# Kernel tuning notes

Measured on AMD Instinct MI355X. Metric: run time of the kernel, lower is better.

## Reference

```python
import jax, jax.numpy as jnp
import numpy as np

T, B, E, H, F = 1024, 2, 1024, 16, 8
D = E // H
R = 2 * T - 1  # relative positions T-1 .. -(T-1)


def setup_inputs() -> dict:
    key = jax.random.key(0)
    ks = jax.random.split(key, 11)
    std = float(np.sqrt(2.0 / (E + E)))
    return {
        "input": jax.random.normal(ks[0], (T, B, E), jnp.float32),
        "pos": jax.random.normal(ks[1], (R, B, E), jnp.float32),
        "factor": jax.random.normal(ks[2], (F,), jnp.float32),
        "in_proj_weight": jax.random.normal(ks[3], (3 * E * E, F), jnp.float32) * std,
        "pos_proj_weight": jax.random.normal(ks[4], (E * E, F), jnp.float32) * std,
        "out_proj_weight": jax.random.normal(ks[5], (E * E, F), jnp.float32) * std,
        "in_proj_bias": jax.random.normal(ks[6], (3 * E, F), jnp.float32) * 0.02,
        "pos_proj_bias": jax.random.normal(ks[7], (E, F), jnp.float32) * 0.02,
        "out_proj_bias": jax.random.normal(ks[8], (E, F), jnp.float32) * 0.02,
        "r_w_bias": jax.random.normal(ks[9], (E, F), jnp.float32) * 0.02,
        "r_r_bias": jax.random.normal(ks[10], (E, F), jnp.float32) * 0.02,
    }


def _rel_shift(x):
    # x: [BH, T, R] -> out[b, i, j] = x[b, i, j + (T-1) - i]
    bh, q, r = x.shape
    zp = jnp.zeros((bh, q, 1), x.dtype)
    xp = jnp.concatenate([zp, x], axis=2).reshape(bh, r + 1, q)
    return xp[:, 1:, :].reshape(bh, q, r)


def reference(input, pos, factor, in_proj_weight, pos_proj_weight, out_proj_weight,
              in_proj_bias, pos_proj_bias, out_proj_bias, r_w_bias, r_r_bias):
    # hypernetwork: generate effective weights from factor vector (torch.mv)
    W_in = (in_proj_weight @ factor).reshape(3 * E, E)
    W_pos = (pos_proj_weight @ factor).reshape(E, E)
    W_out = (out_proj_weight @ factor).reshape(E, E)
    b_in = in_proj_bias @ factor
    b_pos = pos_proj_bias @ factor
    b_out = out_proj_bias @ factor
    rw = (r_w_bias @ factor).reshape(H, D)  # content bias
    rr = (r_r_bias @ factor).reshape(H, D)  # position bias

    qkv = input @ W_in.T + b_in                      # [T, B, 3E]
    q, k, v = jnp.split(qkv, 3, axis=-1)
    q = q.reshape(T, B, H, D)
    k = k.reshape(T, B, H, D)
    v = v.reshape(T, B, H, D)
    r = (pos @ W_pos.T + b_pos).reshape(R, B, H, D)  # [R, B, H, D]

    scale = 1.0 / np.sqrt(D)
    # AC: content-content + content bias term
    AC = jnp.einsum('ibhd,jbhd->bhij', q + rw, k)    # [B, H, T, T]
    # BD: content-position + position bias term, then relative shift
    BD = jnp.einsum('ibhd,rbhd->bhir', q + rr, r)    # [B, H, T, R]
    BD = _rel_shift(BD.reshape(B * H, T, R))[:, :, :T].reshape(B, H, T, T)

    attn = jax.nn.softmax((AC + BD) * scale, axis=-1)  # [B, H, T, T]
    out = jnp.einsum('bhij,jbhd->ibhd', attn, v).reshape(T, B, E)
    out = out @ W_out.T + b_out                       # [T, B, E]
    return out
```

## Files before the change

kernel.cpp:

```cpp
#include <hip/hip_runtime.h>


typedef _Float16 h16;
typedef _Float16 h16x8 __attribute__((ext_vector_type(8)));
typedef _Float16 h16x4 __attribute__((ext_vector_type(4)));
typedef float f32x4 __attribute__((ext_vector_type(4)));

static __device__ __forceinline__ f32x4 mfma16(h16x8 a, h16x8 b, f32x4 c) {
  return __builtin_amdgcn_mfma_f32_16x16x32_f16(a, b, c, 0, 0, 0);
}
static __device__ __forceinline__ void gload16(const void* g, void* l) {
  __builtin_amdgcn_global_load_lds((const __attribute__((address_space(1))) void*)g,
                                   (__attribute__((address_space(3))) void*)l, 16, 0, 0);
}

__global__ __launch_bounds__(256, 2) void hypernet_kernel(
    const float* __restrict__ fac,
    const float* __restrict__ w_in, const float* __restrict__ w_pos,
    const float* __restrict__ w_out, const float* __restrict__ b_in_w,
    const float* __restrict__ b_pos_w, const float* __restrict__ b_out_w,
    const float* __restrict__ rw_w, const float* __restrict__ rr_w,
    h16* __restrict__ Wall,
    float* __restrict__ bin, float* __restrict__ bpos, float* __restrict__ bout,
    float* __restrict__ rw, float* __restrict__ rr, h16* __restrict__ rb,
    const float* __restrict__ input, const float* __restrict__ pos,
    h16* __restrict__ cast_h)
{
  const int tid = threadIdx.x;
  const float f0=fac[0],f1=fac[1],f2=fac[2],f3=fac[3],
              f4=fac[4],f5=fac[5],f6=fac[6],f7=fac[7];
#define DOT(a,b) ((a).x*f0+(a).y*f1+(a).z*f2+(a).w*f3+(b).x*f4+(b).y*f5+(b).z*f6+(b).w*f7)

  if (blockIdx.x < 1280) {
    const int b = blockIdx.x;
    const float* tbl; size_t rowbase;
    if (b < 768)       { tbl = w_in;  rowbase = (size_t)b*4096; }
    else if (b < 1024) { tbl = w_pos; rowbase = (size_t)b*4096 - 3145728; }
    else               { tbl = w_out; rowbase = (size_t)b*4096 - 4194304; }
    const size_t outbase = (size_t)b*4096;
    float4 cur[4], nxt[4];
    {
      const float4* p0 = reinterpret_cast<const float4*>(tbl + (rowbase + tid)*8);
      const float4* p1 = reinterpret_cast<const float4*>(tbl + (rowbase + 256 + tid)*8);
      cur[0]=p0[0]; cur[1]=p0[1]; cur[2]=p1[0]; cur[3]=p1[1];
    }
#pragma unroll
    for (int s = 0; s < 8; ++s) {
      if (s < 7) {
        const float4* p0 = reinterpret_cast<const float4*>(tbl + (rowbase + (s+1)*512 + tid)*8);
        const float4* p1 = reinterpret_cast<const float4*>(tbl + (rowbase + (s+1)*512 + 256 + tid)*8);
        nxt[0]=p0[0]; nxt[1]=p0[1]; nxt[2]=p1[0]; nxt[3]=p1[1];
      }
      Wall[outbase + s*512 + tid]       = (h16)DOT(cur[0], cur[1]);
      Wall[outbase + s*512 + 256 + tid] = (h16)DOT(cur[2], cur[3]);
#pragma unroll
      for (int q = 0; q < 4; ++q) cur[q] = nxt[q];
    }
    return;
  }
  if (blockIdx.x < 1316) {
    int idx = (blockIdx.x - 1280) * 256 + tid;
    if (idx < 3072) {
      const float4* s = reinterpret_cast<const float4*>(b_in_w + (size_t)idx*8);
      bin[idx] = DOT(s[0], s[1]); return;
    }
    idx -= 3072;
    if (idx < 1024) {
      const float4* s = reinterpret_cast<const float4*>(b_pos_w + (size_t)idx*8);
      bpos[idx] = DOT(s[0], s[1]); return;
    }
    idx -= 1024;
    if (idx < 1024) {
      const float4* s = reinterpret_cast<const float4*>(b_out_w + (size_t)idx*8);
      bout[idx] = DOT(s[0], s[1]); return;
    }
    idx -= 1024;
    if (idx < 1024) {
      const float4* s = reinterpret_cast<const float4*>(rw_w + (size_t)idx*8);
      rw[idx] = DOT(s[0], s[1]); return;
    }
    idx -= 1024;
    if (idx < 1024) {
      const float4* s = reinterpret_cast<const float4*>(rr_w + (size_t)idx*8);
      rr[idx] = DOT(s[0], s[1]); return;
    }
    idx -= 1024;
    if (idx < 2048)
      rb[(((size_t)(idx >> 6)) << 17) + 2047*64 + (idx & 63)] = (h16)0.f;
    return;
  }
  {
    const int g = (blockIdx.x - 1316) * 256 + tid;
    float4 v = (g < 524288) ? reinterpret_cast<const float4*>(input)[g]
                            : reinterpret_cast<const float4*>(pos)[g - 524288];
    h16x4 o = { (h16)v.x, (h16)v.y, (h16)v.z, (h16)v.w };
    reinterpret_cast<h16x4*>(cast_h)[g] = o;
  }
#undef DOT
}

template <int MODE>
__global__ __launch_bounds__(256) void gemm_lds_kernel(
    const h16* __restrict__ A, const h16* __restrict__ Bw,
    const float* __restrict__ bias, int M, int N, int K,
    float* __restrict__ Cout,
    const float* __restrict__ rwv, const float* __restrict__ rrv,
    h16* __restrict__ o0, h16* __restrict__ o1,
    h16* __restrict__ o2, h16* __restrict__ o3)
{
  __shared__ __align__(16) h16 a_sm[128*64];
  __shared__ __align__(16) h16 b_sm[128*64];
  const int tid = threadIdx.x, lane = tid & 63, wave = tid >> 6;
  const int quad = lane >> 4, t16 = lane & 15;
  const int wm = wave >> 1, wn = wave & 1;
  const int m0 = blockIdx.y * 128, n0 = blockIdx.x * 128;
  const int lrow = lane >> 3, lgran = lane & 7;
  const int gsw = (lgran ^ lrow) * 8;
  const int xg0 = (quad ^ (t16 & 7)) * 8;
  const int xg1 = xg0 ^ 32;

  f32x4 acc[4][4];
#pragma unroll
  for (int i = 0; i < 4; ++i)
#pragma unroll
    for (int j = 0; j < 4; ++j) acc[i][j] = (f32x4){0.f,0.f,0.f,0.f};

  for (int k0 = 0; k0 < K; k0 += 64) {
    __syncthreads();
#pragma unroll
    for (int s = 0; s < 4; ++s) {
      int rbase = wave*32 + s*8;
      gload16(A  + (size_t)(m0 + rbase + lrow)*K + k0 + gsw, a_sm + rbase*64);
      gload16(Bw + (size_t)(n0 + rbase + lrow)*K + k0 + gsw, b_sm + rbase*64);
    }
    __syncthreads();
#pragma unroll
    for (int kc = 0; kc < 2; ++kc) {
      const int xg = kc ? xg1 : xg0;
      h16x8 af[4], bfr[4];
#pragma unroll
      for (int i = 0; i < 4; ++i) {
        af[i]  = *reinterpret_cast<const h16x8*>(a_sm + (wm*64 + i*16 + t16)*64 + xg);
        bfr[i] = *reinterpret_cast<const h16x8*>(b_sm + (wn*64 + i*16 + t16)*64 + xg);
      }
#pragma unroll
      for (int i = 0; i < 4; ++i)
#pragma unroll
        for (int j = 0; j < 4; ++j)
          acc[i][j] = mfma16(af[i], bfr[j], acc[i][j]);
    }
  }

#pragma unroll
  for (int i = 0; i < 4; ++i) {
    int mb = m0 + wm*64 + i*16 + quad*4;
#pragma unroll
    for (int j = 0; j < 4; ++j) {
      int n = n0 + wn*64 + j*16 + t16;
      float bv = bias[n];
      if (MODE == 2) {
#pragma unroll
        for (int r = 0; r < 4; ++r)
          Cout[(size_t)(mb + r)*N + n] = acc[i][j][r] + bv;
      } else if (MODE == 0) {
        int nn = n & 1023, sec = n >> 10, hh = nn >> 6, d = nn & 63;
        float rwb = rwv[nn], rrb = rrv[nn];
#pragma unroll
        for (int r = 0; r < 4; ++r) {
          int m = mb + r, t = m >> 1, b = m & 1;
          size_t off = ((size_t)((b << 4) + hh) << 16) + (t << 6) + d;
          float v = acc[i][j][r] + bv;
          if (sec == 0)      { o0[off] = (h16)(v + rwb); o1[off] = (h16)(v + rrb); }
          else if (sec == 1) { o2[off] = (h16)v; }
          else               { o3[off] = (h16)v; }
        }
      } else {
        int hh = n >> 6, d = n & 63;
#pragma unroll
        for (int r = 0; r < 4; ++r) {
          int m = mb + r;
          if (m < M) {
            int rel = m >> 1, b = m & 1;
            o0[(((size_t)((b << 4) + hh)) << 17) + (rel << 6) + d] = (h16)(acc[i][j][r] + bv);
          }
        }
      }
    }
  }
}

__global__ __launch_bounds__(256) void transpose_v_kernel(
    const h16* __restrict__ vb, h16* __restrict__ vbt)
{
  __shared__ h16 tile[64*72];
  const int bh = blockIdx.y, t0 = blockIdx.x * 64;
  const int r = threadIdx.x >> 3, c = (threadIdx.x & 7) * 8;
  const h16* src = vb + ((size_t)bh << 16) + (size_t)(t0 + r)*64 + c;
  *reinterpret_cast<h16x8*>(tile + r*72 + c)        = *reinterpret_cast<const h16x8*>(src);
  *reinterpret_cast<h16x8*>(tile + (r + 32)*72 + c) = *reinterpret_cast<const h16x8*>(src + 32*64);
  __syncthreads();
  h16x8 o0, o1;
#pragma unroll
  for (int e = 0; e < 8; ++e) {
    o0[e] = tile[(c + e)*72 + r];
    o1[e] = tile[(c + e)*72 + r + 32];
  }
  h16* dst = vbt + ((size_t)bh << 16) + (size_t)r*1024 + t0 + c;
  *reinterpret_cast<h16x8*>(dst)            = o0;
  *reinterpret_cast<h16x8*>(dst + 32*1024)  = o1;
}

__global__ __launch_bounds__(256) void flash_kernel(
    const h16* __restrict__ qrw, const h16* __restrict__ qrr,
    const h16* __restrict__ kb, const h16* __restrict__ vbt,
    const h16* __restrict__ rb,
    float* __restrict__ o_part, float* __restrict__ ml_part)
{
  __shared__ __align__(16) h16 k_sm[64*64];
  __shared__ __align__(16) h16 vt_sm[64*64];
  __shared__ __align__(16) h16 r_sm[128*64];

  const int tid = threadIdx.x, lane = tid & 63, wave = tid >> 6;
  const int quad = lane >> 4, t16 = lane & 15;
  const int bh = blockIdx.y, i0 = blockIdx.x * 64, jh = blockIdx.z;
  const size_t base  = (size_t)bh << 16;
  const size_t rbase = (size_t)bh << 17;
  const int iw = i0 + wave * 16;
  const int lrow = lane >> 3, lgran = lane & 7;
  const int gsw = (lgran ^ lrow) * 8;
  const int xg0 = (quad ^ (t16 & 7)) * 8;
  const int xg1 = xg0 ^ 32;

  h16x8 a_rw[2], a_rr[2];
  {
    const h16* p = qrw + base + (size_t)(iw + t16)*64 + quad*8;
    a_rw[0] = *reinterpret_cast<const h16x8*>(p);
    a_rw[1] = *reinterpret_cast<const h16x8*>(p + 32);
    const h16* p2 = qrr + base + (size_t)(iw + t16)*64 + quad*8;
    a_rr[0] = *reinterpret_cast<const h16x8*>(p2);
    a_rr[1] = *reinterpret_cast<const h16x8*>(p2 + 32);
  }

  f32x4 o_acc[4];
#pragma unroll
  for (int dc = 0; dc < 4; ++dc) o_acc[dc] = (f32x4){0.f,0.f,0.f,0.f};
  float m_run[4] = {-1e30f,-1e30f,-1e30f,-1e30f};
  float l_run[4] = {0.f,0.f,0.f,0.f};

  h16* bdw = r_sm + wave * (16*84);
  const int cb0 = 3 - wave;

  for (int j0 = jh*256; j0 < jh*256 + 256; j0 += 64) {
    __syncthreads();
    {
#pragma unroll
      for (int s = 0; s < 2; ++s) {
        int row = wave*16 + s*8;
        gload16(kb  + base + (size_t)(j0 + row + lrow)*64 + gsw, k_sm  + row*64);
        gload16(vbt + base + (size_t)(row + lrow)*1024 + j0 + gsw, vt_sm + row*64);
      }
      const int rel0 = j0 - i0 + 960;
#pragma unroll
      for (int s = 0; s < 4; ++s) {
        int row = wave*32 + s*8;
        gload16(rb + rbase + (size_t)(rel0 + row + lrow)*64 + gsw, r_sm + row*64);
      }
    }
    __syncthreads();

    f32x4 s_ac[4];
#pragma unroll
    for (int c = 0; c < 4; ++c) {
      s_ac[c] = (f32x4){0.f,0.f,0.f,0.f};
      s_ac[c] = mfma16(a_rw[0], *reinterpret_cast<const h16x8*>(k_sm + (c*16 + t16)*64 + xg0), s_ac[c]);
      s_ac[c] = mfma16(a_rw[1], *reinterpret_cast<const h16x8*>(k_sm + (c*16 + t16)*64 + xg1), s_ac[c]);
    }
    f32x4 s_bd[5];
#pragma unroll
    for (int u = 0; u < 5; ++u) {
      s_bd[u] = (f32x4){0.f,0.f,0.f,0.f};
      s_bd[u] = mfma16(a_rr[0], *reinterpret_cast<const h16x8*>(r_sm + ((cb0+u)*16 + t16)*64 + xg0), s_bd[u]);
      s_bd[u] = mfma16(a_rr[1], *reinterpret_cast<const h16x8*>(r_sm + ((cb0+u)*16 + t16)*64 + xg1), s_bd[u]);
    }
    __syncthreads();

#pragma unroll
    for (int u = 0; u < 5; ++u)
#pragma unroll
      for (int r = 0; r < 4; ++r)
        bdw[(quad*4 + r)*84 + u*16 + t16] = (h16)s_bd[u][r];

    float sv[4][4];
#pragma unroll
    for (int c = 0; c < 4; ++c)
#pragma unroll
      for (int r = 0; r < 4; ++r) {
        int il = quad*4 + r;
        float bdv = (float)bdw[il*84 + c*16 + t16 + 15 - il];
        sv[c][r] = (s_ac[c][r] + bdv) * 0.125f;
      }

    float alpha[4];
#pragma unroll
    for (int r = 0; r < 4; ++r) {
      float v = fmaxf(fmaxf(sv[0][r], sv[1][r]), fmaxf(sv[2][r], sv[3][r]));
#pragma unroll
      for (int off = 1; off < 16; off <<= 1) v = fmaxf(v, __shfl_xor(v, off, 64));
      float mn = fmaxf(m_run[r], v);
      alpha[r] = __expf(m_run[r] - mn);
      m_run[r] = mn;
    }
#pragma unroll
    for (int r = 0; r < 4; ++r) {
      float s0 = 0.f;
#pragma unroll
      for (int c = 0; c < 4; ++c) {
        float p = __expf(sv[c][r] - m_run[r]);
        sv[c][r] = p; s0 += p;
      }
      l_run[r] = l_run[r]*alpha[r] + s0;
    }
#pragma unroll
    for (int dc = 0; dc < 4; ++dc) {
      f32x4 t = o_acc[dc];
#pragma unroll
      for (int r = 0; r < 4; ++r) t[r] *= alpha[r];
      o_acc[dc] = t;
    }
    h16* pw = bdw;
#pragma unroll
    for (int c = 0; c < 4; ++c)
#pragma unroll
      for (int r = 0; r < 4; ++r)
        pw[(quad*4 + r)*72 + c*16 + t16] = (h16)sv[c][r];

    h16x8 ap0 = *reinterpret_cast<const h16x8*>(pw + t16*72 + quad*8);
    h16x8 ap1 = *reinterpret_cast<const h16x8*>(pw + t16*72 + 32 + quad*8);
#pragma unroll
    for (int dc = 0; dc < 4; ++dc) {
      h16x8 bv0 = *reinterpret_cast<const h16x8*>(vt_sm + (dc*16 + t16)*64 + xg0);
      h16x8 bv1 = *reinterpret_cast<const h16x8*>(vt_sm + (dc*16 + t16)*64 + xg1);
      o_acc[dc] = mfma16(ap0, bv0, o_acc[dc]);
      o_acc[dc] = mfma16(ap1, bv1, o_acc[dc]);
    }
  }

#pragma unroll
  for (int r = 0; r < 4; ++r) {
    float l = l_run[r];
#pragma unroll
    for (int off = 1; off < 16; off <<= 1) l += __shfl_xor(l, off, 64);
    l_run[r] = l;
  }
  const size_t obase = ((size_t)jh*32 + bh) * 1024 * 64;
#pragma unroll
  for (int r = 0; r < 4; ++r) {
    int i = iw + quad*4 + r;
#pragma unroll
    for (int dc = 0; dc < 4; ++dc)
      o_part[obase + (size_t)i*64 + dc*16 + t16] = o_acc[dc][r];
    if (t16 == 0) {
      size_t mo = (((size_t)jh*32 + bh)*1024 + i)*2;
      ml_part[mo]     = m_run[r];
      ml_part[mo + 1] = l_run[r];
    }
  }
}

__global__ __launch_bounds__(256) void combine_kernel(
    const float* __restrict__ o_part, const float* __restrict__ ml_part,
    h16* __restrict__ attn_h)
{
  int gid = blockIdx.x * 256 + threadIdx.x;
  int row = gid >> 4;
  int d4 = (gid & 15) * 4;
  float m[4], l[4];
#pragma unroll
  for (int p = 0; p < 4; ++p) {
    m[p] = ml_part[p*65536 + row*2];
    l[p] = ml_part[p*65536 + row*2 + 1];
  }
  float M = fmaxf(fmaxf(m[0], m[1]), fmaxf(m[2], m[3]));
  float e[4], den = 0.f;
#pragma unroll
  for (int p = 0; p < 4; ++p) { e[p] = __expf(m[p] - M); den += e[p]*l[p]; }
  float inv = 1.f / den;
  float4 acc = {0.f,0.f,0.f,0.f};
#pragma unroll
  for (int p = 0; p < 4; ++p) {
    float4 O = *reinterpret_cast<const float4*>(o_part + (size_t)p*2097152 + (size_t)row*64 + d4);
    acc.x += e[p]*O.x; acc.y += e[p]*O.y; acc.z += e[p]*O.z; acc.w += e[p]*O.w;
  }
  int bh = row >> 10, i = row & 1023, b = bh >> 4, h = bh & 15;
  h16x4 o = { (h16)(acc.x*inv), (h16)(acc.y*inv), (h16)(acc.z*inv), (h16)(acc.w*inv) };
  *reinterpret_cast<h16x4*>(attn_h + ((size_t)(i*2 + b))*1024 + h*64 + d4) = o;
}

extern "C" void kernel_launch(void* const* d_in, const int* in_sizes, int n_in,
                              void* d_out, int out_size, void* d_ws, size_t ws_size,
                              hipStream_t stream)
{
  const float* input  = (const float*)d_in[0];
  const float* pos    = (const float*)d_in[1];
  const float* fac    = (const float*)d_in[2];
  const float* w_in   = (const float*)d_in[3];
  const float* w_pos  = (const float*)d_in[4];
  const float* w_out  = (const float*)d_in[5];
  const float* bin_w  = (const float*)d_in[6];
  const float* bpos_w = (const float*)d_in[7];
  const float* bout_w = (const float*)d_in[8];
  const float* rw_w   = (const float*)d_in[9];
  const float* rr_w   = (const float*)d_in[10];
  float* out = (float*)d_out;
  (void)in_sizes; (void)n_in; (void)out_size; (void)ws_size;

  char* w = (char*)d_ws;
  auto take = [&](size_t bytes) { char* p = w; w += bytes; return p; };
  h16*   Win    = (h16*)take(3145728ull*2);
  h16*   Wpos   = (h16*)take(1048576ull*2);
  h16*   Wout   = (h16*)take(1048576ull*2);
  float* bin    = (float*)take(3072*4);
  float* bpos   = (float*)take(1024*4);
  float* bout   = (float*)take(1024*4);
  float* rw     = (float*)take(1024*4);
  float* rr     = (float*)take(1024*4);
  h16*   in_h   = (h16*)take(2097152ull*2);
  h16*   pos_h  = (h16*)take(4192256ull*2);
  h16*   qrwb   = (h16*)take(2097152ull*2);
  h16*   qrrb   = (h16*)take(2097152ull*2);
  h16*   kb     = (h16*)take(2097152ull*2);
  h16*   vb     = (h16*)take(2097152ull*2);
  h16*   vbt    = (h16*)take(2097152ull*2);
  h16*   rb     = (h16*)take(4194304ull*2);
  float* o_part = (float*)take(4ull*2097152ull*4);
  float* ml     = (float*)take(4ull*65536ull*4);
  h16*   attn_h = (h16*)take(2097152ull*2);

  hypernet_kernel<<<7458, 256, 0, stream>>>(fac, w_in, w_pos, w_out, bin_w, bpos_w, bout_w,
                                            rw_w, rr_w, Win, bin, bpos, bout,
                                            rw, rr, rb, input, pos, in_h);
  gemm_lds_kernel<0><<<dim3(24, 16), 256, 0, stream>>>(in_h, Win, bin, 2048, 3072, 1024,
                                                       nullptr, rw, rr, qrwb, qrrb, kb, vb);
  gemm_lds_kernel<1><<<dim3(8, 32), 256, 0, stream>>>(pos_h, Wpos, bpos, 4094, 1024, 1024,
                                                      nullptr, nullptr, nullptr, rb, nullptr, nullptr, nullptr);
  transpose_v_kernel<<<dim3(16, 32), 256, 0, stream>>>(vb, vbt);
  flash_kernel<<<dim3(16, 32, 4), 256, 0, stream>>>(qrwb, qrrb, kb, vbt, rb, o_part, ml);
  combine_kernel<<<2048, 256, 0, stream>>>(o_part, ml, attn_h);
  gemm_lds_kernel<2><<<dim3(8, 16), 256, 0, stream>>>(attn_h, Wout, bout, 2048, 1024, 1024,
                                                      out, nullptr, nullptr, nullptr, nullptr, nullptr, nullptr);
}
```

Measured before the change: 364.2 us.

## Split hypernet weight generation into separate kernel with LDS double-buffered global loads

Moves the large factorized weight contraction (5M rows x 8 factors) out of the combined prep kernel into its own kernel. The new kernel uses global_load_lds to stream contiguous rows into a per-wave LDS double buffer and writes 4 fp16 outputs per lane. The goal is better-coalesced reads of the 168MB weight tables and more bytes in flight. In exchange it adds an extra kernel launch and fewer blocks (640), with hardcoded waitcnt encodings that must match the count of outstanding loads.

Result: slower. 377.2 us (+3.6%).

```diff
diff --git a/kernel.cpp b/kernel.cpp
--- a/kernel.cpp
+++ b/kernel.cpp
@@ -14,13 +14,11 @@
                                    (__attribute__((address_space(3))) void*)l, 16, 0, 0);
 }
 
-__global__ __launch_bounds__(256, 2) void hypernet_kernel(
+__global__ __launch_bounds__(256) void prep_kernel(
     const float* __restrict__ fac,
-    const float* __restrict__ w_in, const float* __restrict__ w_pos,
-    const float* __restrict__ w_out, const float* __restrict__ b_in_w,
-    const float* __restrict__ b_pos_w, const float* __restrict__ b_out_w,
-    const float* __restrict__ rw_w, const float* __restrict__ rr_w,
-    h16* __restrict__ Wall,
+    const float* __restrict__ b_in_w, const float* __restrict__ b_pos_w,
+    const float* __restrict__ b_out_w, const float* __restrict__ rw_w,
+    const float* __restrict__ rr_w,
     float* __restrict__ bin, float* __restrict__ bpos, float* __restrict__ bout,
     float* __restrict__ rw, float* __restrict__ rr, h16* __restrict__ rb,
     const float* __restrict__ input, const float* __restrict__ pos,
@@ -30,36 +28,8 @@
   const float f0=fac[0],f1=fac[1],f2=fac[2],f3=fac[3],
               f4=fac[4],f5=fac[5],f6=fac[6],f7=fac[7];
 #define DOT(a,b) ((a).x*f0+(a).y*f1+(a).z*f2+(a).w*f3+(b).x*f4+(b).y*f5+(b).z*f6+(b).w*f7)
-
-  if (blockIdx.x < 1280) {
-    const int b = blockIdx.x;
-    const float* tbl; size_t rowbase;
-    if (b < 768)       { tbl = w_in;  rowbase = (size_t)b*4096; }
-    else if (b < 1024) { tbl = w_pos; rowbase = (size_t)b*4096 - 3145728; }
-    else               { tbl = w_out; rowbase = (size_t)b*4096 - 4194304; }
-    const size_t outbase = (size_t)b*4096;
-    float4 cur[4], nxt[4];
-    {
-      const float4* p0 = reinterpret_cast<const float4*>(tbl + (rowbase + tid)*8);
-      const float4* p1 = reinterpret_cast<const float4*>(tbl + (rowbase + 256 + tid)*8);
-      cur[0]=p0[0]; cur[1]=p0[1]; cur[2]=p1[0]; cur[3]=p1[1];
-    }
-#pragma unroll
-    for (int s = 0; s < 8; ++s) {
-      if (s < 7) {
-        const float4* p0 = reinterpret_cast<const float4*>(tbl + (rowbase + (s+1)*512 + tid)*8);
-        const float4* p1 = reinterpret_cast<const float4*>(tbl + (rowbase + (s+1)*512 + 256 + tid)*8);
-        nxt[0]=p0[0]; nxt[1]=p0[1]; nxt[2]=p1[0]; nxt[3]=p1[1];
-      }
-      Wall[outbase + s*512 + tid]       = (h16)DOT(cur[0], cur[1]);
-      Wall[outbase + s*512 + 256 + tid] = (h16)DOT(cur[2], cur[3]);
-#pragma unroll
-      for (int q = 0; q < 4; ++q) cur[q] = nxt[q];
-    }
-    return;
-  }
-  if (blockIdx.x < 1316) {
-    int idx = (blockIdx.x - 1280) * 256 + tid;
+  if (blockIdx.x < 36) {
+    int idx = blockIdx.x * 256 + tid;
     if (idx < 3072) {
       const float4* s = reinterpret_cast<const float4*>(b_in_w + (size_t)idx*8);
       bin[idx] = DOT(s[0], s[1]); return;
@@ -90,13 +60,60 @@
     return;
   }
   {
-    const int g = (blockIdx.x - 1316) * 256 + tid;
+    const int g = (blockIdx.x - 36) * 256 + tid;
     float4 v = (g < 524288) ? reinterpret_cast<const float4*>(input)[g]
                             : reinterpret_cast<const float4*>(pos)[g - 524288];
     h16x4 o = { (h16)v.x, (h16)v.y, (h16)v.z, (h16)v.w };
     reinterpret_cast<h16x4*>(cast_h)[g] = o;
   }
 #undef DOT
+}
+
+__global__ __launch_bounds__(256, 2) void hypernet_kernel(
+    const float* __restrict__ fac,
+    const float* __restrict__ w_in, const float* __restrict__ w_pos,
+    const float* __restrict__ w_out, h16* __restrict__ Wall)
+{
+  __shared__ __align__(16) float lds[16384];
+  const int tid = threadIdx.x, lane = tid & 63, wave = tid >> 6;
+  const float f0=fac[0],f1=fac[1],f2=fac[2],f3=fac[3],
+              f4=fac[4],f5=fac[5],f6=fac[6],f7=fac[7];
+  const int b = blockIdx.x;
+  const float* tbl; size_t rowloc;
+  if (b < 384)      { tbl = w_in;  rowloc = (size_t)b*8192; }
+  else if (b < 512) { tbl = w_pos; rowloc = (size_t)b*8192 - 3145728; }
+  else              { tbl = w_out; rowloc = (size_t)b*8192 - 4194304; }
+  float* wlds = lds + wave*4096;
+  const float* wsrc = tbl + (rowloc + wave*256)*8;
+  h16* wout = Wall + (size_t)b*8192 + wave*256;
+
+#pragma unroll
+  for (int j = 0; j < 8; ++j)
+    gload16(wsrc + (size_t)lane*32 + j*4, wlds + j*256);
+
+  for (int c = 0; c < 8; ++c) {
+    if (c < 7) {
+      const float* csrc = wsrc + (size_t)(c+1)*8192;
+      float* nbuf = wlds + ((c+1) & 1)*2048;
+#pragma unroll
+      for (int j = 0; j < 8; ++j)
+        gload16(csrc + (size_t)lane*32 + j*4, nbuf + j*256);
+      __builtin_amdgcn_s_waitcnt(0xF78);
+    } else {
+      __builtin_amdgcn_s_waitcnt(0xF70);
+    }
+    const float* cbuf = wlds + (c & 1)*2048;
+    float acc[4];
+#pragma unroll
+    for (int s = 0; s < 8; ++s) {
+      f32x4 v = *reinterpret_cast<const f32x4*>(cbuf + s*256 + lane*4);
+      int i = s >> 1;
+      if ((s & 1) == 0) acc[i]  = v[0]*f0 + v[1]*f1 + v[2]*f2 + v[3]*f3;
+      else              acc[i] += v[0]*f4 + v[1]*f5 + v[2]*f6 + v[3]*f7;
+    }
+    h16x4 o = { (h16)acc[0], (h16)acc[1], (h16)acc[2], (h16)acc[3] };
+    *reinterpret_cast<h16x4*>(wout + (size_t)c*1024 + lane*4) = o;
+  }
 }
 
 template <int MODE>
@@ -436,9 +453,9 @@
   float* ml     = (float*)take(4ull*65536ull*4);
   h16*   attn_h = (h16*)take(2097152ull*2);
 
-  hypernet_kernel<<<7458, 256, 0, stream>>>(fac, w_in, w_pos, w_out, bin_w, bpos_w, bout_w,
-                                            rw_w, rr_w, Win, bin, bpos, bout,
-                                            rw, rr, rb, input, pos, in_h);
+  prep_kernel<<<6178, 256, 0, stream>>>(fac, bin_w, bpos_w, bout_w, rw_w, rr_w,
+                                        bin, bpos, bout, rw, rr, rb, input, pos, in_h);
+  hypernet_kernel<<<640, 256, 0, stream>>>(fac, w_in, w_pos, w_out, Win);
   gemm_lds_kernel<0><<<dim3(24, 16), 256, 0, stream>>>(in_h, Win, bin, 2048, 3072, 1024,
                                                        nullptr, rw, rr, qrwb, qrrb, kb, vb);
   gemm_lds_kernel<1><<<dim3(8, 32), 256, 0, stream>>>(pos_h, Wpos, bpos, 4094, 1024, 1024,
```
